# Performance work log

Hardware: AMD Instinct MI355X
Metric: run time of the kernel (lower is better)

## Reference

```python
import jax, jax.numpy as jnp
import numpy as np

B, C, H, W = 32, 1536, 24, 24
HID, D, K = 512, 128, 64  # hidden, cluster_dim, num_clusters


def setup_inputs() -> dict:
    key = jax.random.key(0)
    ks = jax.random.split(key, 6)
    def rn(k, shape, scale):
        return jax.random.normal(k, shape, dtype=jnp.float32) * scale
    return {
        "x": rn(ks[0], (B, C, H, W), 1.0),
        # cluster_features: Conv2d(C,512,1) -> ReLU -> Conv2d(512,D,1)
        "w1c": rn(ks[1], (HID, C), 0.02), "b1c": jnp.zeros((HID,), jnp.float32),
        "w2c": rn(ks[2], (D, HID), 0.02), "b2c": jnp.zeros((D,), jnp.float32),
        # score: Conv2d(C,512,1) -> ReLU -> Conv2d(512,K,1)
        "w1s": rn(ks[3], (HID, C), 0.02), "b1s": jnp.zeros((HID,), jnp.float32),
        "w2s": rn(ks[4], (K, HID), 0.02), "b2s": jnp.zeros((K,), jnp.float32),
        "temperature": jnp.array(1.0, jnp.float32),
    }


def _sinkhorn_log(S, num_iters=3):
    # log-domain OT solver with uniform marginals log(1/n), reg=1 (M/reg == M)
    b, m, n = S.shape
    norm = -jnp.log(jnp.asarray(n, S.dtype))
    log_a = jnp.full((b, m), norm, S.dtype)
    log_b = jnp.full((b, n), norm, S.dtype)
    u = jnp.zeros((b, m), S.dtype)
    v = jnp.zeros((b, n), S.dtype)
    for _ in range(num_iters):
        u = log_a - jax.nn.logsumexp(S + v[:, None, :], axis=2)
        v = log_b - jax.nn.logsumexp(S + u[:, :, None], axis=1)
    # get_matching_probs subtracts norm at the end
    return S + u[:, :, None] + v[:, None, :] - norm


def reference(x, w1c, b1c, w2c, b2c, w1s, b1s, w2s, b2s, temperature):
    b, c, h, w = x.shape
    xf = x.reshape(b, c, h * w)  # (B, C, N); 1x1 conv == channel GEMM
    # cluster features f: (B, D, N)
    hc = jax.nn.relu(jnp.einsum('oc,bcn->bon', w1c, xf) + b1c[None, :, None])
    f = jnp.einsum('oc,bcn->bon', w2c, hc) + b2c[None, :, None]
    # assignment scores p: (B, K, N)
    hs = jax.nn.relu(jnp.einsum('oc,bcn->bon', w1s, xf) + b1s[None, :, None])
    s = jnp.einsum('oc,bcn->bon', w2s, hs) + b2s[None, :, None]
    log_p = _sinkhorn_log(s, num_iters=3)
    p = jnp.exp(log_p / temperature) + jnp.exp(log_p)  # (B, K, N)
    # (f.unsqueeze(2) * p.unsqueeze(1)).sum(-1) == batched matmul
    agg = jnp.einsum('bcn,bkn->bck', f, p)  # (B, D, K)
    flat = agg.reshape(b, -1)
    nrm = jnp.maximum(jnp.linalg.norm(flat, axis=-1, keepdims=True), 1e-12)
    return flat / nrm
```

## Files before the change

kernel.cpp:

```cpp
#include <hip/hip_runtime.h>

typedef unsigned short ushort_t;
typedef float f32x4 __attribute__((ext_vector_type(4)));
typedef short short8 __attribute__((ext_vector_type(8)));

#define B_   32
#define C_   1536
#define N_   576
#define HID_ 512
#define D_   128
#define K_   64

__device__ __forceinline__ float bf2f(ushort_t u) {
    union { unsigned u; float f; } c; c.u = ((unsigned)u) << 16; return c.f;
}
__device__ __forceinline__ ushort_t f2bf(float x) {
    unsigned u = __float_as_uint(x);
    return (ushort_t)((u + 0x7FFFu + ((u >> 16) & 1u)) >> 16);
}

typedef const __attribute__((address_space(1))) char gas_char;
typedef __attribute__((address_space(3))) char las_char;
__device__ __forceinline__ void cp16(const void* g, void* l) {
    __builtin_amdgcn_global_load_lds((gas_char*)(size_t)g,
                                     (las_char*)(unsigned)(size_t)l, 16, 0, 0);
}
__device__ __forceinline__ void bar() {
    asm volatile("" ::: "memory");
    __builtin_amdgcn_s_barrier();
    asm volatile("" ::: "memory");
}

#define OB1_  1572864
#define OW2C_ 1573888
#define OB2C_ 1639424
#define OW2S_ 1639552
#define OB2S_ 1672320
#define WTOT_ 1672384
#define TRB2_ 3456
#define CVB4_ (((WTOT_ / 4) + 255) / 256)

__global__ __launch_bounds__(256) void prep_kernel(
    const void* __restrict__ x,
    const void* __restrict__ w1c, const void* __restrict__ b1c,
    const void* __restrict__ w2c, const void* __restrict__ b2c,
    const void* __restrict__ w1s, const void* __restrict__ b1s,
    const void* __restrict__ w2s, const void* __restrict__ b2s,
    const unsigned* __restrict__ temp,
    ushort_t* __restrict__ xt, ushort_t* __restrict__ o, float* __restrict__ Tp)
{
    __shared__ ushort_t t[128][65];
    unsigned d = temp[0];
    int flag = (d == 0x3F800000u) ? 1 : 0;
    int tid = threadIdx.x;
    int idx = blockIdx.x;
    if (idx == 0 && tid == 0)
        *Tp = flag ? __uint_as_float(d) : bf2f((ushort_t)(d & 0xFFFFu));

    if (idx < TRB2_) {
        int b = idx / 108, rem = idx % 108;
        int c0 = (rem % 12) * 128, n0 = (rem / 12) * 64;
        ushort_t* xtb = xt + (size_t)b * N_ * C_;
        int r = tid >> 4, n4 = (tid & 15) * 4;
        if (flag) {
            const float* xb = (const float*)x + (size_t)b * C_ * N_;
#pragma unroll
            for (int i = 0; i < 8; ++i) {
                int cc = r + i * 16;
                float4 v = *(const float4*)&xb[(size_t)(c0 + cc) * N_ + n0 + n4];
                t[cc][n4 + 0] = f2bf(v.x);
                t[cc][n4 + 1] = f2bf(v.y);
                t[cc][n4 + 2] = f2bf(v.z);
                t[cc][n4 + 3] = f2bf(v.w);
            }
        } else {
            const ushort_t* xb = (const ushort_t*)x + (size_t)b * C_ * N_;
#pragma unroll
            for (int i = 0; i < 8; ++i) {
                int cc = r + i * 16;
                *(uint2*)&t[cc][n4] =
                    *(const uint2*)&xb[(size_t)(c0 + cc) * N_ + n0 + n4];
            }
        }
        __syncthreads();
        int c8 = (tid & 15) * 8;
#pragma unroll
        for (int i = 0; i < 4; ++i) {
            int nn = r + i * 16;
            ushort_t vv[8];
#pragma unroll
            for (int j = 0; j < 8; ++j) vv[j] = t[c8 + j][nn];
            uint4 o4;
            o4.x = (unsigned)vv[0] | ((unsigned)vv[1] << 16);
            o4.y = (unsigned)vv[2] | ((unsigned)vv[3] << 16);
            o4.z = (unsigned)vv[4] | ((unsigned)vv[5] << 16);
            o4.w = (unsigned)vv[6] | ((unsigned)vv[7] << 16);
            *(uint4*)&xtb[(size_t)(n0 + nn) * C_ + c0 + c8] = o4;
        }
    } else {
        int i4 = ((idx - TRB2_) * 256 + tid) * 4;
        if (i4 >= WTOT_) return;
        const void* p; int off;
        if      (i4 < 786432)  { p = w1c; off = i4; }
        else if (i4 < OB1_)    { p = w1s; off = i4 - 786432; }
        else if (i4 < 1573376) { p = b1c; off = i4 - OB1_; }
        else if (i4 < OW2C_)   { p = b1s; off = i4 - 1573376; }
        else if (i4 < OB2C_)   { p = w2c; off = i4 - OW2C_; }
        else if (i4 < OW2S_)   { p = b2c; off = i4 - OB2C_; }
        else if (i4 < OB2S_)   { p = w2s; off = i4 - OW2S_; }
        else                   { p = b2s; off = i4 - OB2S_; }
        if (flag) {
            float4 v = *(const float4*)((const float*)p + off);
            uint2 r;
            r.x = (unsigned)f2bf(v.x) | ((unsigned)f2bf(v.y) << 16);
            r.y = (unsigned)f2bf(v.z) | ((unsigned)f2bf(v.w) << 16);
            *(uint2*)&o[i4] = r;
        } else {
            *(uint2*)&o[i4] = *(const uint2*)((const ushort_t*)p + off);
        }
    }
}

__global__ __launch_bounds__(256) void gemm1_kernel(
    const ushort_t* __restrict__ Xt, const ushort_t* __restrict__ W1,
    const ushort_t* __restrict__ bias, ushort_t* __restrict__ h)
{
    __shared__ ushort_t Atile[2][128 * 64];
    __shared__ ushort_t Btile[2][128 * 64];
    int idx = blockIdx.x;
    int l = (idx & 7) * 144 + (idx >> 3);
    int mt = l >> 3, t = l & 7;
    int row0 = mt * 128, col0 = t * 128;

    int tid = threadIdx.x, w = tid >> 6, lane = tid & 63;
    int wr = w >> 1, wc = w & 1;
    int r16 = lane & 15, q = lane >> 4, kh = q * 8;

    int srow = tid >> 3;
    int cx = ((tid & 7) ^ (srow & 7)) * 8;
    const ushort_t* ag[4];
    const ushort_t* bg[4];
#pragma unroll
    for (int s = 0; s < 4; ++s) {
        ag[s] = Xt + (size_t)(row0 + s * 32 + srow) * C_ + cx;
        bg[s] = W1 + (size_t)(col0 + s * 32 + srow) * C_ + cx;
    }

    f32x4 acc[4][4];
#pragma unroll
    for (int i = 0; i < 4; ++i)
#pragma unroll
        for (int j = 0; j < 4; ++j) acc[i][j] = f32x4{0.f, 0.f, 0.f, 0.f};

    int rowa = wr * 64 + r16;
    int rowb = wc * 64 + r16;
    int xr = (r16 & 7) * 8;

    auto stage = [&](int buf) {
#pragma unroll
        for (int s = 0; s < 4; ++s) {
            cp16(ag[s], &Atile[buf][tid * 8 + s * 2048]);
            cp16(bg[s], &Btile[buf][tid * 8 + s * 2048]);
            ag[s] += 64; bg[s] += 64;
        }
    };
    auto compute = [&](int cb) {
#pragma unroll
        for (int ks = 0; ks < 2; ++ks) {
            int ke = (ks * 32 + kh) ^ xr;
            short8 af[4], bf[4];
#pragma unroll
            for (int i = 0; i < 4; ++i)
                af[i] = *(const short8*)&Atile[cb][(rowa + i * 16) * 64 + ke];
#pragma unroll
            for (int j = 0; j < 4; ++j)
                bf[j] = *(const short8*)&Btile[cb][(rowb + j * 16) * 64 + ke];
#pragma unroll
            for (int i = 0; i < 4; ++i)
#pragma unroll
                for (int j = 0; j < 4; ++j)
                    acc[i][j] = __builtin_amdgcn_mfma_f32_16x16x32_bf16(
                        af[i], bf[j], acc[i][j], 0, 0, 0);
        }
    };

    stage(0);
    int cur = 0;
    for (int kt = 0; kt < 23; ++kt) {
        stage(cur ^ 1);
        asm volatile("s_waitcnt vmcnt(8)" ::: "memory");
        bar();
        compute(cur);
        bar();
        cur ^= 1;
    }
    asm volatile("s_waitcnt vmcnt(0)" ::: "memory");
    bar();
    compute(cur);

#pragma unroll
    for (int j = 0; j < 4; ++j) {
        int col = col0 + wc * 64 + j * 16 + r16;
        float cb = bf2f(bias[col]);
#pragma unroll
        for (int i = 0; i < 4; ++i) {
            int rowo = row0 + wr * 64 + i * 16 + q * 4;
#pragma unroll
            for (int r = 0; r < 4; ++r) {
                float v = fmaxf(acc[i][j][r] + cb, 0.f);
                h[(size_t)(rowo + r) * 1024 + col] = f2bf(v);
            }
        }
    }
}

__global__ __launch_bounds__(256) void gemm2_kernel(
    const ushort_t* __restrict__ Wb, const ushort_t* __restrict__ h,
    ushort_t* __restrict__ fbuf, float* __restrict__ sbuf)
{
    __shared__ ushort_t Atile[2][64 * 32];
    __shared__ ushort_t Btile[2][128 * 32];
    int nt = blockIdx.x, b = blockIdx.y, z = blockIdx.z;
    int col0 = nt * 128;
    const ushort_t* Aw   = Wb + (z == 2 ? OW2S_ : OW2C_ + z * 64 * HID_);
    const ushort_t* bias = Wb + (z == 2 ? OB2S_ : OB2C_ + z * 64);
    const ushort_t* hb = h + (size_t)b * N_ * 1024 + (z == 2 ? 512 : 0);

    int tid = threadIdx.x, w = tid >> 6, lane = tid & 63;
    int wr = w >> 1, wc = w & 1;
    int r16 = lane & 15, q = lane >> 4, kh = q * 8;

    int srow = tid >> 2;
    int swz = ((tid & 3) ^ (srow & 3)) * 8;
    const ushort_t* ag0 = Aw + (size_t)srow * HID_ + swz;
    int br0 = min(col0 + srow, N_ - 1);
    int br1 = min(col0 + 64 + srow, N_ - 1);
    const ushort_t* bg0 = hb + (size_t)br0 * 1024 + swz;
    const ushort_t* bg1 = hb + (size_t)br1 * 1024 + swz;

    f32x4 acc[2][4];
#pragma unroll
    for (int i = 0; i < 2; ++i)
#pragma unroll
        for (int j = 0; j < 4; ++j) acc[i][j] = f32x4{0.f, 0.f, 0.f, 0.f};

    int xr = (r16 & 3) * 8;

    auto stage = [&](int buf) {
        cp16(ag0, &Atile[buf][tid * 8]);
        cp16(bg0, &Btile[buf][tid * 8]);
        cp16(bg1, &Btile[buf][2048 + tid * 8]);
        ag0 += 32; bg0 += 32; bg1 += 32;
    };
    auto compute = [&](int cb) {
        int ke = kh ^ xr;
        short8 af[2], bf[4];
#pragma unroll
        for (int i = 0; i < 2; ++i)
            af[i] = *(const short8*)&Atile[cb][(wr * 32 + i * 16 + r16) * 32 + ke];
#pragma unroll
        for (int j = 0; j < 4; ++j)
            bf[j] = *(const short8*)&Btile[cb][(wc * 64 + j * 16 + r16) * 32 + ke];
#pragma unroll
        for (int i = 0; i < 2; ++i)
#pragma unroll
            for (int j = 0; j < 4; ++j)
                acc[i][j] = __builtin_amdgcn_mfma_f32_16x16x32_bf16(
                    af[i], bf[j], acc[i][j], 0, 0, 0);
    };

    stage(0);
    int cur = 0;
    for (int kt = 0; kt < 15; ++kt) {
        stage(cur ^ 1);
        asm volatile("s_waitcnt vmcnt(3)" ::: "memory");
        bar();
        compute(cur);
        bar();
        cur ^= 1;
    }
    asm volatile("s_waitcnt vmcnt(0)" ::: "memory");
    bar();
    compute(cur);

#pragma unroll
    for (int j = 0; j < 4; ++j) {
        int col = col0 + wc * 64 + j * 16 + r16;
        if (col >= N_) continue;
#pragma unroll
        for (int i = 0; i < 2; ++i) {
            int rowb = wr * 32 + i * 16 + q * 4;
#pragma unroll
            for (int r = 0; r < 4; ++r) {
                int rr = rowb + r;
                float v = acc[i][j][r] + bf2f(bias[rr]);
                if (z == 2)
                    sbuf[(size_t)b * K_ * N_ + (size_t)rr * N_ + col] = v;
                else
                    fbuf[(size_t)b * D_ * N_ +
                         (size_t)(z * 64 + rr) * N_ + col] = f2bf(v);
            }
        }
    }
}

__global__ __launch_bounds__(512) void tail_kernel(
    const ushort_t* __restrict__ f_all, const float* __restrict__ s_all,
    const float* __restrict__ Tp, const unsigned* __restrict__ temp,
    void* __restrict__ out)
{
    __shared__ float Sl[K_ * 577];
    __shared__ float su[K_];
    __shared__ float sv[N_];
    __shared__ float red[8];
    ushort_t* Plds = (ushort_t*)Sl;
    ushort_t* At0  = (ushort_t*)((char*)Sl + 81920);
    ushort_t* At1  = (ushort_t*)((char*)Sl + 81920 + 16384);

    int b = blockIdx.x;
    int tid = threadIdx.x, w = tid >> 6, lane = tid & 63;
    const float norm = -logf((float)N_);

    const float4* S4 = (const float4*)(s_all + (size_t)b * K_ * N_);
    for (int g = tid; g < (K_ * N_) / 4; g += 512) {
        float4 v = S4[g];
        int w0 = g * 4;
        int r = w0 / N_;
        int base = w0 + r;
        Sl[base + 0] = v.x; Sl[base + 1] = v.y;
        Sl[base + 2] = v.z; Sl[base + 3] = v.w;
    }
    for (int n = tid; n < N_; n += 512) sv[n] = 0.f;
    __syncthreads();

    for (int it = 0; it < 3; ++it) {
        for (int r = w; r < K_; r += 8) {
            const float* Sr = Sl + r * 577;
            float a0 = 0.f, a1 = 0.f, a2 = 0.f;
#pragma unroll
            for (int k = 0; k < 9; k += 3) {
                int n0 = lane + 64 * k;
                a0 += __expf(Sr[n0] + sv[n0]);
                a1 += __expf(Sr[n0 + 64] + sv[n0 + 64]);
                a2 += __expf(Sr[n0 + 128] + sv[n0 + 128]);
            }
            float t = a0 + a1 + a2;
#pragma unroll
            for (int off = 32; off; off >>= 1) t += __shfl_xor(t, off);
            if (lane == 0) su[r] = norm - __logf(t);
        }
        __syncthreads();
        for (int n = tid; n < N_; n += 512) {
            const float* Sc = Sl + n;
            float a0 = 0.f, a1 = 0.f, a2 = 0.f, a3 = 0.f;
#pragma unroll
            for (int m = 0; m < K_; m += 4) {
                a0 += __expf(Sc[(m + 0) * 577] + su[m + 0]);
                a1 += __expf(Sc[(m + 1) * 577] + su[m + 1]);
                a2 += __expf(Sc[(m + 2) * 577] + su[m + 2]);
                a3 += __expf(Sc[(m + 3) * 577] + su[m + 3]);
            }
            sv[n] = norm - __logf((a0 + a1) + (a2 + a3));
        }
        __syncthreads();
    }

    float invT = 1.f / (*Tp);
    ushort_t pv[8][9];
#pragma unroll
    for (int rr = 0; rr < 8; ++rr) {
        int r = w * 8 + rr;
        float ur = su[r];
        const float* Sr = Sl + r * 577;
#pragma unroll
        for (int k = 0; k < 9; ++k) {
            int n0 = lane + 64 * k;
            float lp = Sr[n0] + ur + sv[n0] - norm;
            pv[rr][k] = f2bf(__expf(lp * invT) + __expf(lp));
        }
    }
    __syncthreads();
#pragma unroll
    for (int rr = 0; rr < 8; ++rr) {
        int r = w * 8 + rr;
#pragma unroll
        for (int k = 0; k < 9; ++k)
            Plds[r * 584 + lane + 64 * k] = pv[rr][k];
    }
    __syncthreads();

    int wr = w >> 2, wc = w & 3;
    int r16 = lane & 15, q = lane >> 4, kh = q * 8;
    const ushort_t* F = f_all + (size_t)b * D_ * N_;
    int srow = tid >> 3;
    int cx = ((tid & 7) ^ (srow & 7)) * 8;
    const ushort_t* fg0 = F + (size_t)srow * N_ + cx;
    const ushort_t* fg1 = F + (size_t)(64 + srow) * N_ + cx;

    f32x4 acc[4];
#pragma unroll
    for (int i = 0; i < 4; ++i) acc[i] = f32x4{0.f, 0.f, 0.f, 0.f};

    int rowa = wr * 64 + r16;
    int prow = wc * 16 + r16;
    int xr = (r16 & 7) * 8;

    auto stageF = [&](ushort_t* At, int koff) {
        cp16(fg0 + koff, At + tid * 8);
        cp16(fg1 + koff, At + 4096 + tid * 8);
    };
    auto computeT = [&](const ushort_t* At, int s) {
#pragma unroll
        for (int ks = 0; ks < 2; ++ks) {
            int ke = (ks * 32 + kh) ^ xr;
            short8 af[4];
#pragma unroll
            for (int i = 0; i < 4; ++i)
                af[i] = *(const short8*)&At[(rowa + i * 16) * 64 + ke];
            short8 pf = *(const short8*)&Plds[prow * 584 + s * 64 + ks * 32 + kh];
#pragma unroll
            for (int i = 0; i < 4; ++i)
                acc[i] = __builtin_amdgcn_mfma_f32_16x16x32_bf16(
                    af[i], pf, acc[i], 0, 0, 0);
        }
    };

    stageF(At0, 0);
#pragma unroll
    for (int kt = 0; kt < 9; ++kt) {
        ushort_t* cb = (kt & 1) ? At1 : At0;
        ushort_t* nb = (kt & 1) ? At0 : At1;
        if (kt < 8) {
            stageF(nb, (kt + 1) * 64);
            asm volatile("s_waitcnt vmcnt(2)" ::: "memory");
        } else {
            asm volatile("s_waitcnt vmcnt(0)" ::: "memory");
        }
        bar();
        computeT(cb, kt);
        bar();
    }

    float ssq = 0.f;
#pragma unroll
    for (int i = 0; i < 4; ++i)
#pragma unroll
        for (int r = 0; r < 4; ++r) { float v = acc[i][r]; ssq += v * v; }
#pragma unroll
    for (int off = 32; off; off >>= 1) ssq += __shfl_xor(ssq, off);
    if (lane == 0) red[w] = ssq;
    __syncthreads();
    float tot = (red[0] + red[1] + red[2] + red[3])
              + (red[4] + red[5] + red[6] + red[7]);
    float inv = 1.f / fmaxf(sqrtf(tot), 1e-12f);
    int flag = (temp[0] == 0x3F800000u) ? 1 : 0;
#pragma unroll
    for (int i = 0; i < 4; ++i) {
        int col = wc * 16 + r16;
#pragma unroll
        for (int r = 0; r < 4; ++r) {
            int row = wr * 64 + i * 16 + q * 4 + r;
            float v = acc[i][r] * inv;
            size_t idx = (size_t)b * D_ * K_ + (size_t)row * K_ + col;
            if (flag) ((float*)out)[idx] = v;
            else      ((ushort_t*)out)[idx] = f2bf(v);
        }
    }
}

extern "C" void kernel_launch(void* const* d_in, const int* in_sizes, int n_in,
                              void* d_out, int out_size, void* d_ws, size_t ws_size,
                              hipStream_t stream) {
    const void* x    = d_in[0];
    const void* w1c  = d_in[1];
    const void* b1c  = d_in[2];
    const void* w2c  = d_in[3];
    const void* b2c  = d_in[4];
    const void* w1s  = d_in[5];
    const void* b1s  = d_in[6];
    const void* w2s  = d_in[7];
    const void* b2s  = d_in[8];
    const unsigned* temp = (const unsigned*)d_in[9];

    char* ws = (char*)d_ws;
    float* Tp = (float*)ws;
    ushort_t* Wb = (ushort_t*)(ws + 256);
    size_t offXt = 256 + (((size_t)WTOT_ * 2 + 255) & ~(size_t)255);
    ushort_t* Xt = (ushort_t*)(ws + offXt);
    size_t xtBytes = (size_t)B_ * N_ * C_ * 2;
    ushort_t* h  = (ushort_t*)(ws + offXt + xtBytes);
    size_t o0 = offXt;
    ushort_t* fbuf = (ushort_t*)(ws + o0);  o0 += (size_t)B_ * D_ * N_ * 2;
    float*    sbuf = (float*)(ws + o0);     o0 += (size_t)B_ * K_ * N_ * 4;

    prep_kernel<<<dim3(TRB2_ + CVB4_), 256, 0, stream>>>(
        x, w1c, b1c, w2c, b2c, w1s, b1s, w2s, b2s, temp, Xt, Wb, Tp);
    gemm1_kernel<<<dim3(1152), 256, 0, stream>>>(Xt, Wb, Wb + OB1_, h);
    gemm2_kernel<<<dim3(5, B_, 3), 256, 0, stream>>>(Wb, h, fbuf, sbuf);
    tail_kernel<<<dim3(B_), 512, 0, stream>>>(fbuf, sbuf, Tp, temp, (void*)d_out);
}
```

Before: 300.4 us.

## Halve gemm1 K-tile to 32 and widen weight conversion to 8 elements

The first GEMM's K tile drops from 64 to 32, which halves LDS usage per block (64KB to 32KB) and doubles the K-loop trip count, with the swizzle rebuilt for 4 chunks per row. The aim is more resident blocks per CU and better latency hiding, paid for with twice as many barriers per unit of work. Separately, the weight-conversion part of prep now handles 8 elements per thread with 16-byte stores, using fewer blocks.

Result: slower. 311.9 us (+3.8%).

```diff
diff --git a/kernel.cpp b/kernel.cpp
--- a/kernel.cpp
+++ b/kernel.cpp
@@ -38,7 +38,7 @@
 #define OB2S_ 1672320
 #define WTOT_ 1672384
 #define TRB2_ 3456
-#define CVB4_ (((WTOT_ / 4) + 255) / 256)
+#define CVB8_ (((WTOT_ / 8) + 255) / 256)
 
 __global__ __launch_bounds__(256) void prep_kernel(
     const void* __restrict__ x,
@@ -98,25 +98,28 @@
             *(uint4*)&xtb[(size_t)(n0 + nn) * C_ + c0 + c8] = o4;
         }
     } else {
-        int i4 = ((idx - TRB2_) * 256 + tid) * 4;
-        if (i4 >= WTOT_) return;
+        int i8 = ((idx - TRB2_) * 256 + tid) * 8;
+        if (i8 >= WTOT_) return;
         const void* p; int off;
-        if      (i4 < 786432)  { p = w1c; off = i4; }
-        else if (i4 < OB1_)    { p = w1s; off = i4 - 786432; }
-        else if (i4 < 1573376) { p = b1c; off = i4 - OB1_; }
-        else if (i4 < OW2C_)   { p = b1s; off = i4 - 1573376; }
-        else if (i4 < OB2C_)   { p = w2c; off = i4 - OW2C_; }
-        else if (i4 < OW2S_)   { p = b2c; off = i4 - OB2C_; }
-        else if (i4 < OB2S_)   { p = w2s; off = i4 - OW2S_; }
-        else                   { p = b2s; off = i4 - OB2S_; }
+        if      (i8 < 786432)  { p = w1c; off = i8; }
+        else if (i8 < OB1_)    { p = w1s; off = i8 - 786432; }
+        else if (i8 < 1573376) { p = b1c; off = i8 - OB1_; }
+        else if (i8 < OW2C_)   { p = b1s; off = i8 - 1573376; }
+        else if (i8 < OB2C_)   { p = w2c; off = i8 - OW2C_; }
+        else if (i8 < OW2S_)   { p = b2c; off = i8 - OB2C_; }
+        else if (i8 < OB2S_)   { p = w2s; off = i8 - OW2S_; }
+        else                   { p = b2s; off = i8 - OB2S_; }
         if (flag) {
-            float4 v = *(const float4*)((const float*)p + off);
-            uint2 r;
-            r.x = (unsigned)f2bf(v.x) | ((unsigned)f2bf(v.y) << 16);
-            r.y = (unsigned)f2bf(v.z) | ((unsigned)f2bf(v.w) << 16);
-            *(uint2*)&o[i4] = r;
+            float4 v0 = *(const float4*)((const float*)p + off);
+            float4 v1 = *(const float4*)((const float*)p + off + 4);
+            uint4 r;
+            r.x = (unsigned)f2bf(v0.x) | ((unsigned)f2bf(v0.y) << 16);
+            r.y = (unsigned)f2bf(v0.z) | ((unsigned)f2bf(v0.w) << 16);
+            r.z = (unsigned)f2bf(v1.x) | ((unsigned)f2bf(v1.y) << 16);
+            r.w = (unsigned)f2bf(v1.z) | ((unsigned)f2bf(v1.w) << 16);
+            *(uint4*)&o[i8] = r;
         } else {
-            *(uint2*)&o[i4] = *(const uint2*)((const ushort_t*)p + off);
+            *(uint4*)&o[i8] = *(const uint4*)((const ushort_t*)p + off);
         }
     }
 }
@@ -125,8 +128,8 @@
     const ushort_t* __restrict__ Xt, const ushort_t* __restrict__ W1,
     const ushort_t* __restrict__ bias, ushort_t* __restrict__ h)
 {
-    __shared__ ushort_t Atile[2][128 * 64];
-    __shared__ ushort_t Btile[2][128 * 64];
+    __shared__ ushort_t Atile[2][128 * 32];
+    __shared__ ushort_t Btile[2][128 * 32];
     int idx = blockIdx.x;
     int l = (idx & 7) * 144 + (idx >> 3);
     int mt = l >> 3, t = l & 7;
@@ -136,15 +139,12 @@
     int wr = w >> 1, wc = w & 1;
     int r16 = lane & 15, q = lane >> 4, kh = q * 8;
 
-    int srow = tid >> 3;
-    int cx = ((tid & 7) ^ (srow & 7)) * 8;
-    const ushort_t* ag[4];
-    const ushort_t* bg[4];
-#pragma unroll
-    for (int s = 0; s < 4; ++s) {
-        ag[s] = Xt + (size_t)(row0 + s * 32 + srow) * C_ + cx;
-        bg[s] = W1 + (size_t)(col0 + s * 32 + srow) * C_ + cx;
-    }
+    int srow = tid >> 2;
+    int swz = ((tid & 3) ^ (srow & 3)) * 8;
+    const ushort_t* ag0 = Xt + (size_t)(row0 + srow) * C_ + swz;
+    const ushort_t* ag1 = Xt + (size_t)(row0 + 64 + srow) * C_ + swz;
+    const ushort_t* bg0 = W1 + (size_t)(col0 + srow) * C_ + swz;
+    const ushort_t* bg1 = W1 + (size_t)(col0 + 64 + srow) * C_ + swz;
 
     f32x4 acc[4][4];
 #pragma unroll
@@ -154,41 +154,37 @@
 
     int rowa = wr * 64 + r16;
     int rowb = wc * 64 + r16;
-    int xr = (r16 & 7) * 8;
+    int xr = (r16 & 3) * 8;
 
     auto stage = [&](int buf) {
-#pragma unroll
-        for (int s = 0; s < 4; ++s) {
-            cp16(ag[s], &Atile[buf][tid * 8 + s * 2048]);
-            cp16(bg[s], &Btile[buf][tid * 8 + s * 2048]);
-            ag[s] += 64; bg[s] += 64;
-        }
+        cp16(ag0, &Atile[buf][tid * 8]);
+        cp16(ag1, &Atile[buf][2048 + tid * 8]);
+        cp16(bg0, &Btile[buf][tid * 8]);
+        cp16(bg1, &Btile[buf][2048 + tid * 8]);
+        ag0 += 32; ag1 += 32; bg0 += 32; bg1 += 32;
     };
     auto compute = [&](int cb) {
-#pragma unroll
-        for (int ks = 0; ks < 2; ++ks) {
-            int ke = (ks * 32 + kh) ^ xr;
-            short8 af[4], bf[4];
-#pragma unroll
-            for (int i = 0; i < 4; ++i)
-                af[i] = *(const short8*)&Atile[cb][(rowa + i * 16) * 64 + ke];
+        int ke = kh ^ xr;
+        short8 af[4], bf[4];
+#pragma unroll
+        for (int i = 0; i < 4; ++i)
+            af[i] = *(const short8*)&Atile[cb][(rowa + i * 16) * 32 + ke];
+#pragma unroll
+        for (int j = 0; j < 4; ++j)
+            bf[j] = *(const short8*)&Btile[cb][(rowb + j * 16) * 32 + ke];
+#pragma unroll
+        for (int i = 0; i < 4; ++i)
 #pragma unroll
             for (int j = 0; j < 4; ++j)
-                bf[j] = *(const short8*)&Btile[cb][(rowb + j * 16) * 64 + ke];
-#pragma unroll
-            for (int i = 0; i < 4; ++i)
-#pragma unroll
-                for (int j = 0; j < 4; ++j)
-                    acc[i][j] = __builtin_amdgcn_mfma_f32_16x16x32_bf16(
-                        af[i], bf[j], acc[i][j], 0, 0, 0);
-        }
+                acc[i][j] = __builtin_amdgcn_mfma_f32_16x16x32_bf16(
+                    af[i], bf[j], acc[i][j], 0, 0, 0);
     };
 
     stage(0);
     int cur = 0;
-    for (int kt = 0; kt < 23; ++kt) {
+    for (int kt = 0; kt < 47; ++kt) {
         stage(cur ^ 1);
-        asm volatile("s_waitcnt vmcnt(8)" ::: "memory");
+        asm volatile("s_waitcnt vmcnt(4)" ::: "memory");
         bar();
         compute(cur);
         bar();
@@ -493,7 +489,7 @@
     ushort_t* fbuf = (ushort_t*)(ws + o0);  o0 += (size_t)B_ * D_ * N_ * 2;
     float*    sbuf = (float*)(ws + o0);     o0 += (size_t)B_ * K_ * N_ * 4;
 
-    prep_kernel<<<dim3(TRB2_ + CVB4_), 256, 0, stream>>>(
+    prep_kernel<<<dim3(TRB2_ + CVB8_), 256, 0, stream>>>(
         x, w1c, b1c, w2c, b2c, w1s, b1s, w2s, b2s, temp, Xt, Wb, Tp);
     gemm1_kernel<<<dim3(1152), 256, 0, stream>>>(Xt, Wb, Wb + OB1_, h);
     gemm2_kernel<<<dim3(5, B_, 3), 256, 0, stream>>>(Wb, h, fbuf, sbuf);
```
